# Optimization experiments

Measured on AMD Instinct MI355X. Metric: run time of the kernel, lower is better.

Reference implementation:

```python
import jax, jax.numpy as jnp
import numpy as np

V, D, H, L, F, S, B = 32000, 1024, 16, 4, 4096, 1024, 2
THETA = 10000.0
EPS = 1e-5


def rmsnorm(x, w):
    # faithful to source: rms = sqrt(mean(x^2)) + eps (eps OUTSIDE the sqrt)
    rms = jnp.sqrt(jnp.mean(x * x, axis=-1, keepdims=True)) + EPS
    return (x / rms) * w


def rope(x, pos):
    # x: [B, H, S, dk]; rotate interleaved even/odd pairs
    dk = x.shape[-1]
    inv_freq = 1.0 / (THETA ** (jnp.arange(0, dk, 2, dtype=jnp.float32) / dk))
    ang = pos[:, None].astype(jnp.float32) * inv_freq[None, :]  # [S, dk/2]
    cos, sin = jnp.cos(ang), jnp.sin(ang)
    x1, x2 = x[..., ::2], x[..., 1::2]
    r1 = x1 * cos - x2 * sin
    r2 = x1 * sin + x2 * cos
    return jnp.stack([r1, r2], axis=-1).reshape(x.shape)


def setup_inputs() -> dict:
    key = jax.random.key(0)
    ks = jax.random.split(key, 12)
    s_attn = np.sqrt(2.0 / (D + D)).astype(np.float32)
    s_ffn = np.sqrt(2.0 / (F + D)).astype(np.float32)
    s_head = np.sqrt(2.0 / (V + D)).astype(np.float32)
    return {
        "token_ids": jax.random.randint(ks[0], (B, S), 0, V),
        "tok_emb": jax.random.normal(ks[1], (V, D), jnp.float32),
        "lm_head_w": jax.random.normal(ks[2], (V, D), jnp.float32) * s_head,
        "ln_final_w": jnp.ones((D,), jnp.float32),
        "q_w": jax.random.normal(ks[3], (L, D, D), jnp.float32) * s_attn,
        "k_w": jax.random.normal(ks[4], (L, D, D), jnp.float32) * s_attn,
        "v_w": jax.random.normal(ks[5], (L, D, D), jnp.float32) * s_attn,
        "o_w": jax.random.normal(ks[6], (L, D, D), jnp.float32) * s_attn,
        "ln1_w": jnp.ones((L, D), jnp.float32),
        "ln2_w": jnp.ones((L, D), jnp.float32),
        "w1": jax.random.normal(ks[7], (L, F, D), jnp.float32) * s_ffn,
        "w2": jax.random.normal(ks[8], (L, D, F), jnp.float32) * s_ffn,
        "w3": jax.random.normal(ks[9], (L, F, D), jnp.float32) * s_ffn,
    }


def reference(token_ids, tok_emb, lm_head_w, ln_final_w, q_w, k_w, v_w, o_w,
              ln1_w, ln2_w, w1, w2, w3):
    b, s = token_ids.shape
    dk = D // H
    scale = 1.0 / np.sqrt(dk).astype(np.float32)
    pos = jnp.arange(s)
    causal = jnp.tril(jnp.ones((s, s), dtype=bool))  # mask[i,j] = i >= j
    x = tok_emb[token_ids]  # [B, S, D]

    for l in range(L):
        # attention block with RoPE
        h = rmsnorm(x, ln1_w[l])
        q = (h @ q_w[l].T).reshape(b, s, H, dk).transpose(0, 2, 1, 3)
        k = (h @ k_w[l].T).reshape(b, s, H, dk).transpose(0, 2, 1, 3)
        v = (h @ v_w[l].T).reshape(b, s, H, dk).transpose(0, 2, 1, 3)
        q = rope(q, pos)
        k = rope(k, pos)
        scores = jnp.einsum('bhqd,bhkd->bhqk', q, k) * scale
        scores = jnp.where(causal, scores, -jnp.inf)
        attn = jax.nn.softmax(scores, axis=-1)
        o = jnp.einsum('bhqk,bhkd->bhqd', attn, v)
        o = o.transpose(0, 2, 1, 3).reshape(b, s, D)
        x = x + o @ o_w[l].T

        # SwiGLU FFN block
        h2 = rmsnorm(x, ln2_w[l])
        xw = h2 @ w1[l].T                       # [B, S, F]
        swish = xw * jax.nn.sigmoid(xw)
        x = x + (swish * (h2 @ w3[l].T)) @ w2[l].T

    x = rmsnorm(x, ln_final_w)
    return x @ lm_head_w.T  # logits [B, S, V]
```

## Files before the change

kernel.cpp:

```cpp
#include <hip/hip_runtime.h>
#include <math.h>

#define V_SZ 32000
#define D_SZ 1024
#define H_SZ 16
#define L_SZ 4
#define F_SZ 4096
#define S_SZ 1024
#define B_SZ 2
#define DK 64
#define NTOK (B_SZ * S_SZ)
#define NEG_INF -3.0e38f

typedef _Float16 half8 __attribute__((ext_vector_type(8)));
typedef _Float16 half4 __attribute__((ext_vector_type(4)));
typedef float floatx4 __attribute__((ext_vector_type(4)));

__device__ __forceinline__ void gload16(const void* g, void* l) {
    __builtin_amdgcn_global_load_lds(
        (const __attribute__((address_space(1))) unsigned int*)g,
        (__attribute__((address_space(3))) unsigned int*)l, 16, 0, 0);
}

__global__ __launch_bounds__(256) void f2h7(const float* __restrict__ sq,
                                            const float* __restrict__ sk,
                                            const float* __restrict__ sv,
                                            const float* __restrict__ so,
                                            const float* __restrict__ s1,
                                            const float* __restrict__ s3,
                                            const float* __restrict__ s2,
                                            _Float16* __restrict__ d,
                                            int nDD8, int nFD8) {
    const int i = blockIdx.x * 256 + threadIdx.x;
    const float* s;
    int off;
    if (i < 4 * nDD8) {
        const int sel = i / nDD8;
        off = i - sel * nDD8;
        s = sel == 0 ? sq : (sel == 1 ? sk : (sel == 2 ? sv : so));
    } else {
        const int j = i - 4 * nDD8;
        const int sel = j / nFD8;
        off = j - sel * nFD8;
        s = sel == 0 ? s1 : (sel == 1 ? s3 : s2);
    }
    const float4 a = ((const float4*)s)[2 * off];
    const float4 b = ((const float4*)s)[2 * off + 1];
    half8 h = {(_Float16)a.x, (_Float16)a.y, (_Float16)a.z, (_Float16)a.w,
               (_Float16)b.x, (_Float16)b.y, (_Float16)b.z, (_Float16)b.w};
    ((half8*)d)[i] = h;
}

__global__ __launch_bounds__(256) void f2h(const float* __restrict__ in,
                                           _Float16* __restrict__ out, int n8) {
    const int i = blockIdx.x * 256 + threadIdx.x;
    if (i >= n8) return;
    const float4 a = ((const float4*)in)[2 * i];
    const float4 b = ((const float4*)in)[2 * i + 1];
    half8 h = {(_Float16)a.x, (_Float16)a.y, (_Float16)a.z, (_Float16)a.w,
               (_Float16)b.x, (_Float16)b.y, (_Float16)b.z, (_Float16)b.w};
    ((half8*)out)[i] = h;
}

__global__ __launch_bounds__(256) void embed_kernel(const int* __restrict__ ids,
                                                    const float* __restrict__ emb,
                                                    float* __restrict__ x) {
    const int row = blockIdx.x;
    const int id = ids[row];
    const float4* src = (const float4*)(emb + (size_t)id * D_SZ);
    float4* dst = (float4*)(x + (size_t)row * D_SZ);
    dst[threadIdx.x] = src[threadIdx.x];
}

__global__ __launch_bounds__(256) void rmsnorm_kernel(const float* __restrict__ x,
                                                      const float* __restrict__ w,
                                                      _Float16* __restrict__ out) {
    const int row = blockIdx.x;
    const int tid = threadIdx.x;
    const float4 v = ((const float4*)(x + (size_t)row * D_SZ))[tid];
    float ss = v.x * v.x + v.y * v.y + v.z * v.z + v.w * v.w;
#pragma unroll
    for (int off = 32; off > 0; off >>= 1) ss += __shfl_down(ss, off, 64);
    __shared__ float red[4];
    if ((tid & 63) == 0) red[tid >> 6] = ss;
    __syncthreads();
    const float tot = red[0] + red[1] + red[2] + red[3];
    const float inv = 1.0f / (sqrtf(tot * (1.0f / (float)D_SZ)) + 1e-5f);
    const float4 wv = ((const float4*)w)[tid];
    half4 o = {(_Float16)(v.x * inv * wv.x), (_Float16)(v.y * inv * wv.y),
               (_Float16)(v.z * inv * wv.z), (_Float16)(v.w * inv * wv.w)};
    ((half4*)(out + (size_t)row * D_SZ))[tid] = o;
}

template <int EPI, bool MFAST, int TM>
__global__ __launch_bounds__(256) void hgemm(const _Float16* __restrict__ A,
                                             const _Float16* __restrict__ B,
                                             float* __restrict__ Cf,
                                             _Float16* Ch,
                                             const _Float16* AUXh,
                                             _Float16* Cq,
                                             _Float16* Ck,
                                             _Float16* Cv,
                                             int M, int N, int K) {
    constexpr int WN = (TM == 128) ? 2 : 4;
    constexpr int CW = 128 / WN;
    constexpr int FN = CW / 16;
    __shared__ __align__(16) _Float16 As[2][TM * 32];
    __shared__ __align__(16) _Float16 Bs[2][128 * 32];
    const int tid = threadIdx.x;
    const int lane = tid & 63;
    const int wave = tid >> 6;
    const int wr = (TM == 128) ? (wave >> 1) : 0;
    const int wc = (TM == 128) ? (wave & 1) : wave;
    const int l15 = lane & 15, g = lane >> 4;

    const int gm = M / TM, gn = N >> 7, nwg = gm * gn;
    const int orig = blockIdx.x;
    const int q8 = nwg >> 3, r8 = nwg & 7, xcd = orig & 7, j8 = orig >> 3;
    const int wgid = (xcd < r8 ? xcd * (q8 + 1) : r8 * (q8 + 1) + (xcd - r8) * q8) + j8;
    const int bm = MFAST ? (wgid % gm) : (wgid / gn);
    const int bn = MFAST ? (wgid / gm) : (wgid % gn);
    const int m0 = bm * TM, n0 = bn * 128;

    const int offA0 = wave * (TM * 16) + lane * 16;
    const int offA1 = offA0 + 1024;
    const int rA0 = offA0 >> 6, kA0 = offA0 & 63;
    const int rA1 = offA1 >> 6, kA1 = offA1 & 63;
    const int offB0 = wave * 2048 + lane * 16;
    const int offB1 = offB0 + 1024;
    const int rB0 = offB0 >> 6, kB0 = offB0 & 63;
    const int rB1 = offB1 >> 6, kB1 = offB1 & 63;
    const char* gA0 = (const char*)(A + (size_t)(m0 + rA0) * K) + kA0;
    const char* gA1 = (const char*)(A + (size_t)(m0 + rA1) * K) + kA1;
    const char* gB0 = (const char*)(B + (size_t)(n0 + rB0) * K) + kB0;
    const char* gB1 = (const char*)(B + (size_t)(n0 + rB1) * K) + kB1;

#define STAGE(buf)                                                     \
    do {                                                               \
        gload16(gA0, (char*)As[buf] + offA0);                          \
        if constexpr (TM == 128) gload16(gA1, (char*)As[buf] + offA1); \
        gload16(gB0, (char*)Bs[buf] + offB0);                          \
        gload16(gB1, (char*)Bs[buf] + offB1);                          \
        gA0 += 64; gA1 += 64; gB0 += 64; gB1 += 64;                    \
    } while (0)

    floatx4 acc[4][FN];
#pragma unroll
    for (int i = 0; i < 4; i++)
#pragma unroll
        for (int j = 0; j < FN; j++) acc[i][j] = 0;

    STAGE(0);
    __syncthreads();
    int cur = 0;
    for (int kk = 0; kk < K; kk += 32) {
        if (kk + 32 < K) STAGE(cur ^ 1);
        half8 aF[4], bF[FN];
#pragma unroll
        for (int i = 0; i < 4; i++)
            aF[i] = *(const half8*)&As[cur][(wr * 64 + i * 16 + l15) * 32 + g * 8];
#pragma unroll
        for (int j = 0; j < FN; j++)
            bF[j] = *(const half8*)&Bs[cur][(wc * CW + j * 16 + l15) * 32 + g * 8];
#pragma unroll
        for (int i = 0; i < 4; i++)
#pragma unroll
            for (int j = 0; j < FN; j++)
                acc[i][j] = __builtin_amdgcn_mfma_f32_16x16x32_f16(aF[i], bF[j], acc[i][j], 0, 0, 0);
        __syncthreads();
        cur ^= 1;
    }
#undef STAGE

    const int rb = m0 + wr * 64 + g * 4;
    const int cb = n0 + wc * CW + l15;
    if (EPI == 4) {
        const int sel = n0 >> 10;
        _Float16* Cx = sel == 0 ? Cq : (sel == 1 ? Ck : Cv);
        const int cb0 = cb - sel * 1024;
#pragma unroll
        for (int i = 0; i < 4; i++) {
#pragma unroll
            for (int e = 0; e < 4; e++) {
                const int row = rb + i * 16 + e;
                const int pos = row & (S_SZ - 1);
#pragma unroll
                for (int j = 0; j < FN; j++) {
                    float v = acc[i][j][e];
                    const int col = cb0 + j * 16;
                    if (sel < 2) {
                        const float pp = __shfl_xor(v, 1, 64);
                        const int pi = (col & 63) >> 1;
                        const float invf = exp2f((float)pi * -0.41524101186f);
                        float sn, cs;
                        sincosf((float)pos * invf, &sn, &cs);
                        v = (col & 1) ? (pp * sn + v * cs) : (v * cs - pp * sn);
                    }
                    Cx[(size_t)row * 1024 + col] = (_Float16)v;
                }
            }
        }
        return;
    }
#pragma unroll
    for (int i = 0; i < 4; i++) {
#pragma unroll
        for (int e = 0; e < 4; e++) {
            const int row = rb + i * 16 + e;
#pragma unroll
            for (int j = 0; j < FN; j++) {
                const float v = acc[i][j][e];
                const int col = cb + j * 16;
                if (EPI == 0) {
                    Cf[(size_t)row * N + col] = v;
                } else if (EPI == 1) {
                    Cf[(size_t)row * N + col] += v;
                } else if (EPI == 2) {
                    Ch[(size_t)row * N + col] =
                        (_Float16)(v / (1.0f + __expf(-v)));
                } else if (EPI == 3) {
                    const size_t idx = (size_t)row * N + col;
                    Ch[idx] = (_Float16)((float)AUXh[idx] * v);
                }
            }
        }
    }
}

__global__ __launch_bounds__(256) void hgemm_ff(const _Float16* __restrict__ A,
                                                const _Float16* __restrict__ B1,
                                                const _Float16* __restrict__ B3,
                                                _Float16* __restrict__ Ch,
                                                int M, int N, int K) {
    __shared__ __align__(16) _Float16 As[2][64 * 32];
    __shared__ __align__(16) _Float16 Bs1[2][128 * 32];
    __shared__ __align__(16) _Float16 Bs3[2][128 * 32];
    const int tid = threadIdx.x;
    const int lane = tid & 63;
    const int wave = tid >> 6;
    const int l15 = lane & 15, g = lane >> 4;

    const int gm = M >> 6, gn = N >> 7, nwg = gm * gn;
    const int orig = blockIdx.x;
    const int q8 = nwg >> 3, r8 = nwg & 7, xcd = orig & 7, j8 = orig >> 3;
    const int wgid = (xcd < r8 ? xcd * (q8 + 1) : r8 * (q8 + 1) + (xcd - r8) * q8) + j8;
    const int bm = wgid % gm, bn = wgid / gm;
    const int m0 = bm * 64, n0 = bn * 128;

    const int offA = wave * 1024 + lane * 16;
    const int rA = offA >> 6, kA = offA & 63;
    const int offB0 = wave * 2048 + lane * 16;
    const int offB1 = offB0 + 1024;
    const int rB0 = offB0 >> 6, kB0 = offB0 & 63;
    const int rB1 = offB1 >> 6, kB1 = offB1 & 63;
    const char* gA  = (const char*)(A  + (size_t)(m0 + rA) * K) + kA;
    const char* gB10 = (const char*)(B1 + (size_t)(n0 + rB0) * K) + kB0;
    const char* gB11 = (const char*)(B1 + (size_t)(n0 + rB1) * K) + kB1;
    const char* gB30 = (const char*)(B3 + (size_t)(n0 + rB0) * K) + kB0;
    const char* gB31 = (const char*)(B3 + (size_t)(n0 + rB1) * K) + kB1;

#define STAGEF(buf)                                   \
    do {                                              \
        gload16(gA,   (char*)As[buf]  + offA);        \
        gload16(gB10, (char*)Bs1[buf] + offB0);       \
        gload16(gB11, (char*)Bs1[buf] + offB1);       \
        gload16(gB30, (char*)Bs3[buf] + offB0);       \
        gload16(gB31, (char*)Bs3[buf] + offB1);       \
        gA += 64; gB10 += 64; gB11 += 64;             \
        gB30 += 64; gB31 += 64;                       \
    } while (0)

    floatx4 acc1[4][2], acc3[4][2];
#pragma unroll
    for (int i = 0; i < 4; i++)
#pragma unroll
        for (int j = 0; j < 2; j++) { acc1[i][j] = 0; acc3[i][j] = 0; }

    STAGEF(0);
    __syncthreads();
    int cur = 0;
    for (int kk = 0; kk < K; kk += 32) {
        if (kk + 32 < K) STAGEF(cur ^ 1);
        half8 aF[4], b1F[2], b3F[2];
#pragma unroll
        for (int i = 0; i < 4; i++)
            aF[i] = *(const half8*)&As[cur][(i * 16 + l15) * 32 + g * 8];
#pragma unroll
        for (int j = 0; j < 2; j++) {
            b1F[j] = *(const half8*)&Bs1[cur][(wave * 32 + j * 16 + l15) * 32 + g * 8];
            b3F[j] = *(const half8*)&Bs3[cur][(wave * 32 + j * 16 + l15) * 32 + g * 8];
        }
#pragma unroll
        for (int i = 0; i < 4; i++)
#pragma unroll
            for (int j = 0; j < 2; j++) {
                acc1[i][j] = __builtin_amdgcn_mfma_f32_16x16x32_f16(aF[i], b1F[j], acc1[i][j], 0, 0, 0);
                acc3[i][j] = __builtin_amdgcn_mfma_f32_16x16x32_f16(aF[i], b3F[j], acc3[i][j], 0, 0, 0);
            }
        __syncthreads();
        cur ^= 1;
    }
#undef STAGEF

    const int cb = n0 + wave * 32 + l15;
#pragma unroll
    for (int i = 0; i < 4; i++) {
#pragma unroll
        for (int e = 0; e < 4; e++) {
            const int row = m0 + i * 16 + g * 4 + e;
#pragma unroll
            for (int j = 0; j < 2; j++) {
                const float v1 = acc1[i][j][e];
                const float v3 = acc3[i][j][e];
                const float sw = v1 / (1.0f + __expf(-v1));
                Ch[(size_t)row * N + cb + j * 16] = (_Float16)(sw * v3);
            }
        }
    }
}

__global__ __launch_bounds__(256) void vtrans(const _Float16* __restrict__ vh,
                                              _Float16* __restrict__ vt) {
    __shared__ __align__(16) _Float16 Ls[64][80];
    const int t = threadIdx.x;
    const int s0 = blockIdx.x * 64;
    const int bh = blockIdx.y;
    const int b = bh >> 4, h = bh & 15;
#pragma unroll
    for (int p = 0; p < 2; ++p) {
        const int sl = p * 32 + (t >> 3);
        const int d = (t & 7) * 8;
        *(half8*)&Ls[sl][d] =
            *(const half8*)&vh[((size_t)b * S_SZ + s0 + sl) * D_SZ + h * 64 + d];
    }
    __syncthreads();
#pragma unroll
    for (int p = 0; p < 2; ++p) {
        const int d = p * 32 + (t >> 3);
        const int sc = (t & 7) * 8;
        half8 v;
#pragma unroll
        for (int j = 0; j < 8; ++j) v[j] = Ls[sc + j][d];
        *(half8*)&vt[((size_t)bh * 64 + d) * S_SZ + s0 + sc] = v;
    }
}

__global__ __launch_bounds__(256) void attn_mfma(const _Float16* __restrict__ qh,
                                                 const _Float16* __restrict__ kh,
                                                 const _Float16* __restrict__ vt,
                                                 _Float16* __restrict__ o) {
    __shared__ __align__(16) _Float16 Ks[2][64 * 64];
    __shared__ __align__(16) _Float16 Vs[2][64 * 64];
    __shared__ __align__(16) _Float16 Ps[4][16][88];
    const int tid = threadIdx.x;
    const int lane = tid & 63, wave = tid >> 6;
    const int l15 = lane & 15, g = lane >> 4;
    const int bx = blockIdx.x;
    const int bh = blockIdx.y;
    const int h = bh & 15;
    const size_t tokb = (size_t)(bh >> 4) * S_SZ;

    const int qt0 = bx, qt1 = 15 - bx;
    const int qb0 = qt0 * 64, qb1 = qt1 * 64;
    const int ktmax = qt1;

    const int qrow = l15 * 4 + wave;
    half8 qA0[2], qA1[2];
#pragma unroll
    for (int kk = 0; kk < 2; ++kk) {
        qA0[kk] = *(const half8*)&qh[(tokb + qb0 + qrow) * D_SZ + h * 64 + kk * 32 + g * 8];
        qA1[kk] = *(const half8*)&qh[(tokb + qb1 + qrow) * D_SZ + h * 64 + kk * 32 + g * 8];
    }

    floatx4 accO0[4], accO1[4];
#pragma unroll
    for (int s = 0; s < 4; s++) { accO0[s] = 0; accO1[s] = 0; }
    float m0_[4] = {NEG_INF, NEG_INF, NEG_INF, NEG_INF};
    float l0_[4] = {0.0f, 0.0f, 0.0f, 0.0f};
    float m1_[4] = {NEG_INF, NEG_INF, NEG_INF, NEG_INF};
    float l1_[4] = {0.0f, 0.0f, 0.0f, 0.0f};

    const char* KbB = (const char*)(kh + tokb * D_SZ + h * 64);
    const char* VbB = (const char*)(vt + (size_t)bh * 64 * S_SZ);
    const int so0 = wave * 2048 + lane * 16;
    const int so1 = so0 + 1024;
    const int r0 = so0 >> 7, c0 = (so0 >> 4) & 7;
    const int r1 = so1 >> 7, c1 = (so1 >> 4) & 7;
    const int gc0 = ((c0 ^ (r0 & 7)) << 4);
    const int gc1 = ((c1 ^ (r1 & 7)) << 4);

#define STAGEKV(buf, kt)                                                   \
    do {                                                                   \
        const size_t kvr = (size_t)(kt) * 64;                              \
        gload16(KbB + (kvr + r0) * 2048 + gc0, (char*)Ks[buf] + so0);      \
        gload16(KbB + (kvr + r1) * 2048 + gc1, (char*)Ks[buf] + so1);      \
        gload16(VbB + r0 * 2048 + kvr * 2 + gc0, (char*)Vs[buf] + so0);    \
        gload16(VbB + r1 * 2048 + kvr * 2 + gc1, (char*)Vs[buf] + so1);    \
    } while (0)

#define LDSW(arr, rr, cc) \
    (*(const half8*)&(arr)[(rr) * 64 + ((((cc) ^ ((rr) & 7))) << 3)])

    auto computeTile = [&](const half8* qA, floatx4* accO, float* m_, float* l_,
                           int qbase, int kt, bool diag, int buf) {
        const int kv0 = kt * 64;
        floatx4 accS[4];
        __builtin_amdgcn_s_setprio(1);
#pragma unroll
        for (int sub = 0; sub < 4; ++sub) {
            accS[sub] = 0;
#pragma unroll
            for (int kk = 0; kk < 2; ++kk) {
                half8 kB = LDSW(Ks[buf], sub * 16 + l15, kk * 4 + g);
                accS[sub] = __builtin_amdgcn_mfma_f32_16x16x32_f16(qA[kk], kB, accS[sub], 0, 0, 0);
            }
        }
        __builtin_amdgcn_s_setprio(0);
        float sv[4][4];
        float mx[4] = {NEG_INF, NEG_INF, NEG_INF, NEG_INF};
#pragma unroll
        for (int sub = 0; sub < 4; ++sub)
#pragma unroll
            for (int e = 0; e < 4; ++e) {
                float s = accS[sub][e] * 0.125f;
                if (diag && (kv0 + sub * 16 + l15 > qbase + (g * 4 + e) * 4 + wave))
                    s = NEG_INF;
                sv[sub][e] = s;
                mx[e] = fmaxf(mx[e], s);
            }
#pragma unroll
        for (int msk = 1; msk <= 8; msk <<= 1)
#pragma unroll
            for (int e = 0; e < 4; ++e)
                mx[e] = fmaxf(mx[e], __shfl_xor(mx[e], msk, 64));
        float sf[4];
#pragma unroll
        for (int e = 0; e < 4; ++e) {
            const float mn = fmaxf(m_[e], mx[e]);
            sf[e] = __expf(m_[e] - mn);
            m_[e] = mn;
        }
        float rs[4] = {0.0f, 0.0f, 0.0f, 0.0f};
#pragma unroll
        for (int sub = 0; sub < 4; ++sub)
#pragma unroll
            for (int e = 0; e < 4; ++e) {
                const float p = __expf(sv[sub][e] - m_[e]);
                sv[sub][e] = p;
                rs[e] += p;
            }
#pragma unroll
        for (int msk = 1; msk <= 8; msk <<= 1)
#pragma unroll
            for (int e = 0; e < 4; ++e)
                rs[e] += __shfl_xor(rs[e], msk, 64);
#pragma unroll
        for (int e = 0; e < 4; ++e) l_[e] = l_[e] * sf[e] + rs[e];
#pragma unroll
        for (int sub = 0; sub < 4; ++sub)
#pragma unroll
            for (int e = 0; e < 4; ++e) accO[sub][e] *= sf[e];
#pragma unroll
        for (int sub = 0; sub < 4; ++sub)
#pragma unroll
            for (int e = 0; e < 4; ++e)
                Ps[wave][g * 4 + e][sub * 16 + l15] = (_Float16)sv[sub][e];
        half8 aP[2];
        aP[0] = *(const half8*)&Ps[wave][l15][g * 8];
        aP[1] = *(const half8*)&Ps[wave][l15][32 + g * 8];
        __builtin_amdgcn_s_setprio(1);
#pragma unroll
        for (int sub = 0; sub < 4; ++sub)
#pragma unroll
            for (int kk = 0; kk < 2; ++kk) {
                half8 vB = LDSW(Vs[buf], sub * 16 + l15, kk * 4 + g);
                accO[sub] = __builtin_amdgcn_mfma_f32_16x16x32_f16(aP[kk], vB, accO[sub], 0, 0, 0);
            }
        __builtin_amdgcn_s_setprio(0);
    };

    STAGEKV(0, 0);
    __syncthreads();
    int cur = 0;
    for (int kt = 0; kt <= ktmax; ++kt) {
        if (kt < ktmax) STAGEKV(cur ^ 1, kt + 1);
        computeTile(qA1, accO1, m1_, l1_, qb1, kt, kt == qt1, cur);
        if (kt <= qt0)
            computeTile(qA0, accO0, m0_, l0_, qb0, kt, kt == qt0, cur);
        __syncthreads();
        cur ^= 1;
    }
#undef STAGEKV
#undef LDSW

#pragma unroll
    for (int sub = 0; sub < 4; ++sub)
#pragma unroll
        for (int e = 0; e < 4; ++e) {
            const int rr = (g * 4 + e) * 4 + wave;
            o[(tokb + qb1 + rr) * D_SZ + h * 64 + sub * 16 + l15] =
                (_Float16)(accO1[sub][e] / l1_[e]);
            o[(tokb + qb0 + rr) * D_SZ + h * 64 + sub * 16 + l15] =
                (_Float16)(accO0[sub][e] / l0_[e]);
        }
}

extern "C" void kernel_launch(void* const* d_in, const int* in_sizes, int n_in,
                              void* d_out, int out_size, void* d_ws, size_t ws_size,
                              hipStream_t stream) {
    const int*   token_ids  = (const int*)d_in[0];
    const float* tok_emb    = (const float*)d_in[1];
    const float* lm_head_w  = (const float*)d_in[2];
    const float* ln_final_w = (const float*)d_in[3];
    const float* q_w        = (const float*)d_in[4];
    const float* k_w        = (const float*)d_in[5];
    const float* v_w        = (const float*)d_in[6];
    const float* o_w        = (const float*)d_in[7];
    const float* ln1_w      = (const float*)d_in[8];
    const float* ln2_w      = (const float*)d_in[9];
    const float* w1         = (const float*)d_in[10];
    const float* w2         = (const float*)d_in[11];
    const float* w3         = (const float*)d_in[12];
    float* out = (float*)d_out;

    char* W = (char*)d_ws;
    const size_t MB = 1u << 20;
    float*    x    = (float*)(W + 0);
    _Float16* h    = (_Float16*)(W + 8 * MB);
    _Float16* ao   = (_Float16*)(W + 12 * MB);
    _Float16* wq   = (_Float16*)(W + 16 * MB);
    _Float16* wo   = wq + 3 * (1u << 20);
    _Float16* ww1  = (_Float16*)(W + 24 * MB);
    _Float16* ww3  = ww1 + (size_t)F_SZ * D_SZ;
    _Float16* ww2  = ww1 + 2 * (size_t)F_SZ * D_SZ;
    _Float16* qh   = (_Float16*)(W + 48 * MB);
    _Float16* kh   = (_Float16*)(W + 52 * MB);
    _Float16* vh   = (_Float16*)(W + 56 * MB);
    _Float16* vt   = (_Float16*)(W + 60 * MB);
    _Float16* ff1h = (_Float16*)(W + 64 * MB);
    _Float16* whead = (_Float16*)(W + 24 * MB);

    embed_kernel<<<NTOK, 256, 0, stream>>>(token_ids, tok_emb, x);

    const int nDD8 = D_SZ * D_SZ / 8;
    const int nFD8 = F_SZ * D_SZ / 8;
    const int nCNV = 4 * nDD8 + 3 * nFD8;
    const dim3 gQKV(3 * D_SZ / 128 * (NTOK / 128));
    const dim3 gD64(D_SZ / 128 * (NTOK / 64));
    const dim3 gFF(F_SZ / 128 * (NTOK / 64));
    const dim3 gATT(S_SZ / 128, B_SZ * H_SZ);
    const dim3 gVT(S_SZ / 64, B_SZ * H_SZ);

    for (int l = 0; l < L_SZ; l++) {
        const size_t oDD = (size_t)l * D_SZ * D_SZ;
        const size_t oFD = (size_t)l * F_SZ * D_SZ;
        rmsnorm_kernel<<<NTOK, 256, 0, stream>>>(x, ln1_w + (size_t)l * D_SZ, h);
        f2h7<<<nCNV / 256, 256, 0, stream>>>(q_w + oDD, k_w + oDD, v_w + oDD,
                                             o_w + oDD, w1 + oFD, w3 + oFD,
                                             w2 + oFD, wq, nDD8, nFD8);
        hgemm<4, true, 128><<<gQKV, 256, 0, stream>>>(h, wq, nullptr, nullptr, nullptr,
                                                      qh, kh, vh, NTOK, 3 * D_SZ, D_SZ);
        vtrans<<<gVT, 256, 0, stream>>>(vh, vt);
        attn_mfma<<<gATT, 256, 0, stream>>>(qh, kh, vt, ao);
        hgemm<1, false, 64><<<gD64, 256, 0, stream>>>(ao, wo, x, nullptr, nullptr,
                                                      nullptr, nullptr, nullptr, NTOK, D_SZ, D_SZ);
        rmsnorm_kernel<<<NTOK, 256, 0, stream>>>(x, ln2_w + (size_t)l * D_SZ, h);
        hgemm_ff<<<gFF, 256, 0, stream>>>(h, ww1, ww3, ff1h, NTOK, F_SZ, D_SZ);
        hgemm<1, false, 64><<<gD64, 256, 0, stream>>>(ff1h, ww2, x, nullptr, nullptr,
                                                      nullptr, nullptr, nullptr, NTOK, D_SZ, F_SZ);
    }
    rmsnorm_kernel<<<NTOK, 256, 0, stream>>>(x, ln_final_w, h);
    const int nVD8 = V_SZ * D_SZ / 8;
    f2h<<<(nVD8 + 255) / 256, 256, 0, stream>>>(lm_head_w, whead, nVD8);
    const dim3 gOUT(V_SZ / 128 * (NTOK / 128));
    hgemm<0, true, 128><<<gOUT, 256, 0, stream>>>(h, whead, out, nullptr, nullptr,
                                                  nullptr, nullptr, nullptr, NTOK, V_SZ, D_SZ);
}
```

Measured before the change: 1.242 ms.

## Use 256x256-tile 8-wave ping-pong MFMA GEMM for LM head

Adds a new 512-thread GEMM kernel that computes 256x256 output tiles with double-buffered LDS split into two K-halves. Loads are interleaved with MFMA phases behind barriers and raised wave priority, and workgroups are remapped by XCD. It is used only for the final LM-head projection (2048x32000x1024), replacing the 128x128 hgemm. The aim is more data reuse per LDS load and better overlap of global loads with MFMA. In exchange it needs 128KB of LDS per block and more accumulator registers, which lowers occupancy.

New measurement: 1.212 ms. -2.4%, faster.

```diff
diff --git a/kernel.cpp b/kernel.cpp
--- a/kernel.cpp
+++ b/kernel.cpp
@@ -92,6 +92,137 @@
     ((half4*)(out + (size_t)row * D_SZ))[tid] = o;
 }
 
+template <bool MFAST>
+__global__ __launch_bounds__(512) void hgemm8p(const _Float16* __restrict__ A,
+                                               const _Float16* __restrict__ B,
+                                               float* __restrict__ Cf,
+                                               int M, int N, int K) {
+    __shared__ __align__(16) _Float16 As[2][2][256 * 32];
+    __shared__ __align__(16) _Float16 Bs[2][2][256 * 32];
+    const int tid = threadIdx.x;
+    const int lane = tid & 63, wave = tid >> 6;
+    const int wm = wave >> 2, wn = wave & 3;
+    const int l15 = lane & 15, g = lane >> 4;
+
+    const int gm = M >> 8, gn = N >> 8, nwg = gm * gn;
+    const int orig = blockIdx.x;
+    const int q8 = nwg >> 3, r8 = nwg & 7, xcd = orig & 7, j8 = orig >> 3;
+    const int wgid = (xcd < r8 ? xcd * (q8 + 1) : r8 * (q8 + 1) + (xcd - r8) * q8) + j8;
+    const int bm = MFAST ? (wgid % gm) : (wgid / gn);
+    const int bn = MFAST ? (wgid / gm) : (wgid % gn);
+    const int m0 = bm << 8, n0 = bn << 8;
+
+    const int rowS = tid >> 2;
+    const int srcC = ((tid & 3) ^ (rowS & 3)) << 4;
+    const size_t Kb = (size_t)K * 2;
+    const char* gA = (const char*)A + (size_t)(m0 + rowS) * Kb + srcC;
+    const char* gB = (const char*)B + (size_t)(n0 + rowS) * Kb + srcC;
+    const size_t g128 = 128 * Kb;
+
+#define STA(ks, t, buf) do {                                              \
+        const char* _s = gA + (size_t)(t) * 128 + (ks) * 64;              \
+        char* _d = (char*)&As[buf][ks][0];                                \
+        gload16(_s, _d + tid * 16);                                       \
+        gload16(_s + g128, _d + 8192 + tid * 16);                         \
+    } while (0)
+#define STB(ks, t, buf) do {                                              \
+        const char* _s = gB + (size_t)(t) * 128 + (ks) * 64;              \
+        char* _d = (char*)&Bs[buf][ks][0];                                \
+        gload16(_s, _d + tid * 16);                                       \
+        gload16(_s + g128, _d + 8192 + tid * 16);                         \
+    } while (0)
+
+    half8 aF[8], bF[2];
+#define READA(buf, ks) do {                                               \
+        _Pragma("unroll")                                                 \
+        for (int i = 0; i < 8; i++) {                                     \
+            const int R = wm * 128 + i * 16 + l15;                        \
+            aF[i] = *(const half8*)((const char*)&As[buf][ks][0] +        \
+                                    R * 64 + ((g ^ (R & 3)) << 4));       \
+        }                                                                 \
+    } while (0)
+#define READB(buf, ks, nh) do {                                           \
+        _Pragma("unroll")                                                 \
+        for (int jj = 0; jj < 2; jj++) {                                  \
+            const int R = wn * 64 + ((nh) * 2 + jj) * 16 + l15;           \
+            bF[jj] = *(const half8*)((const char*)&Bs[buf][ks][0] +       \
+                                     R * 64 + ((g ^ (R & 3)) << 4));      \
+        }                                                                 \
+    } while (0)
+#define MFMA16(nh) do {                                                   \
+        __builtin_amdgcn_s_setprio(1);                                    \
+        _Pragma("unroll")                                                 \
+        for (int i = 0; i < 8; i++) {                                     \
+            acc[i][(nh) * 2 + 0] = __builtin_amdgcn_mfma_f32_16x16x32_f16(\
+                aF[i], bF[0], acc[i][(nh) * 2 + 0], 0, 0, 0);             \
+            acc[i][(nh) * 2 + 1] = __builtin_amdgcn_mfma_f32_16x16x32_f16(\
+                aF[i], bF[1], acc[i][(nh) * 2 + 1], 0, 0, 0);             \
+        }                                                                 \
+        __builtin_amdgcn_s_setprio(0);                                    \
+    } while (0)
+#define FENCE_MID() do {                                                  \
+        __builtin_amdgcn_s_barrier();                                     \
+        asm volatile("s_waitcnt lgkmcnt(0)" ::: "memory");                \
+        __builtin_amdgcn_sched_barrier(0);                                \
+    } while (0)
+
+    floatx4 acc[8][4];
+#pragma unroll
+    for (int i = 0; i < 8; i++)
+#pragma unroll
+        for (int j = 0; j < 4; j++) acc[i][j] = 0;
+
+    const int nt = K >> 6;
+    STA(0, 0, 0); STB(0, 0, 0); STA(1, 0, 0); STB(1, 0, 0);
+    STA(0, 1, 1); STB(0, 1, 1);
+
+    for (int t = 0; t < nt; ++t) {
+        const int buf = t & 1, nbuf = buf ^ 1;
+        if (t == nt - 1) asm volatile("s_waitcnt vmcnt(0)" ::: "memory");
+        else             asm volatile("s_waitcnt vmcnt(4)" ::: "memory");
+        __builtin_amdgcn_s_barrier();
+        READA(buf, 0); READB(buf, 0, 0);
+        if (t + 1 < nt) STA(1, t + 1, nbuf);
+        FENCE_MID();
+        MFMA16(0);
+        __builtin_amdgcn_s_barrier();
+        READB(buf, 0, 1);
+        if (t + 1 < nt) STB(1, t + 1, nbuf);
+        FENCE_MID();
+        MFMA16(1);
+        __builtin_amdgcn_s_barrier();
+        READA(buf, 1); READB(buf, 1, 0);
+        if (t + 2 < nt) STA(0, t + 2, buf);
+        FENCE_MID();
+        MFMA16(0);
+        __builtin_amdgcn_s_barrier();
+        READB(buf, 1, 1);
+        if (t + 2 < nt) STB(0, t + 2, buf);
+        FENCE_MID();
+        MFMA16(1);
+        __builtin_amdgcn_s_barrier();
+    }
+#undef STA
+#undef STB
+#undef READA
+#undef READB
+#undef MFMA16
+#undef FENCE_MID
+
+#pragma unroll
+    for (int i = 0; i < 8; i++) {
+#pragma unroll
+        for (int e = 0; e < 4; e++) {
+            const int row = m0 + wm * 128 + i * 16 + g * 4 + e;
+#pragma unroll
+            for (int j = 0; j < 4; j++) {
+                const int col = n0 + wn * 64 + j * 16 + l15;
+                Cf[(size_t)row * N + col] = acc[i][j][e];
+            }
+        }
+    }
+}
+
 template <int EPI, bool MFAST, int TM>
 __global__ __launch_bounds__(256) void hgemm(const _Float16* __restrict__ A,
                                              const _Float16* __restrict__ B,
@@ -572,7 +703,6 @@
     rmsnorm_kernel<<<NTOK, 256, 0, stream>>>(x, ln_final_w, h);
     const int nVD8 = V_SZ * D_SZ / 8;
     f2h<<<(nVD8 + 255) / 256, 256, 0, stream>>>(lm_head_w, whead, nVD8);
-    const dim3 gOUT(V_SZ / 128 * (NTOK / 128));
-    hgemm<0, true, 128><<<gOUT, 256, 0, stream>>>(h, whead, out, nullptr, nullptr,
-                                                  nullptr, nullptr, nullptr, NTOK, V_SZ, D_SZ);
-}
+    const dim3 gOUT(V_SZ / 256 * (NTOK / 256));
+    hgemm8p<true><<<gOUT, 512, 0, stream>>>(h, whead, out, NTOK, V_SZ, D_SZ);
+}
```
